# Kernel optimization log

Measured on AMD Instinct MI355X. Metric: run time of the kernel, lower is better.

## Reference

```python
import jax, jax.numpy as jnp
import numpy as np

# Orthonormal (integral-normalized) real spherical harmonics, l = 0..3,
# components ordered [Y_0^0, Y_1^{-1..1}, Y_2^{-2..2}, Y_3^{-3..3}],
# with the e3nn/cuEquivariance l=1 ordering (y, z, x).
_C00 = float(0.5 * np.sqrt(1.0 / np.pi))
_C1 = float(np.sqrt(3.0 / (4.0 * np.pi)))
_C2m2 = float(0.5 * np.sqrt(15.0 / np.pi))
_C20 = float(0.25 * np.sqrt(5.0 / np.pi))
_C22 = float(0.25 * np.sqrt(15.0 / np.pi))
_C3m3 = float(0.25 * np.sqrt(35.0 / (2.0 * np.pi)))
_C3m2 = float(0.5 * np.sqrt(105.0 / np.pi))
_C3m1 = float(0.25 * np.sqrt(21.0 / (2.0 * np.pi)))
_C30 = float(0.25 * np.sqrt(7.0 / np.pi))
_C32 = float(0.25 * np.sqrt(105.0 / np.pi))

N_EDGES = 4_000_000


def setup_inputs() -> dict:
    key = jax.random.key(0)
    vectors = jax.random.normal(key, (N_EDGES, 3), dtype=jnp.float32)
    return {"vectors": vectors}


def _sh_l3(vectors):
    # normalize=True: project onto unit sphere first
    v = vectors * jax.lax.rsqrt(jnp.sum(vectors * vectors, axis=-1, keepdims=True))
    x, y, z = v[..., 0], v[..., 1], v[..., 2]
    x2, y2, z2 = x * x, y * y, z * z
    one = jnp.ones_like(x)
    ys = [
        _C00 * one,                       # l=0
        _C1 * y, _C1 * z, _C1 * x,        # l=1 (m=-1,0,1)
        _C2m2 * x * y,                    # l=2, m=-2
        _C2m2 * y * z,                    # l=2, m=-1
        _C20 * (3.0 * z2 - 1.0),          # l=2, m=0
        _C2m2 * x * z,                    # l=2, m=1
        _C22 * (x2 - y2),                 # l=2, m=2
        _C3m3 * y * (3.0 * x2 - y2),      # l=3, m=-3
        _C3m2 * x * y * z,                # l=3, m=-2
        _C3m1 * y * (5.0 * z2 - 1.0),     # l=3, m=-1
        _C30 * z * (5.0 * z2 - 3.0),      # l=3, m=0
        _C3m1 * x * (5.0 * z2 - 1.0),     # l=3, m=1
        _C32 * z * (x2 - y2),             # l=3, m=2
        _C3m3 * x * (x2 - 3.0 * y2),      # l=3, m=3
    ]
    return jnp.stack(ys, axis=-1)  # (..., 16)


def reference(vectors) -> jnp.ndarray:
    return _sh_l3(vectors)
```

## Files before the change

kernel.cpp:

```cpp
#include <hip/hip_runtime.h>

#define C00  0.28209479177387814f
#define C1   0.4886025119029199f
#define C2M2 1.0925484305920792f
#define C20  0.31539156525252005f
#define C22  0.5462742152960396f
#define C3M3 0.5900435899266435f
#define C3M2 2.890611442640554f
#define C3M1 0.4570457994644658f
#define C30  0.3731763325901154f
#define C32  1.445305721320277f

typedef float vfloat4 __attribute__((ext_vector_type(4)));

#define NBLOCKS 2048

__global__ __launch_bounds__(256) void sh_l3_kernel(
    const float* __restrict__ v, float* __restrict__ out, int ntiles) {
    __shared__ float vin[2][768];

    const int t = threadIdx.x;
    const unsigned c = t & 3u;
    const unsigned esub = t >> 2;

    const vfloat4* v4 = reinterpret_cast<const vfloat4*>(v);
    vfloat4* out4 = reinterpret_cast<vfloat4*>(out);

    unsigned tile = blockIdx.x;
    if (tile < (unsigned)ntiles && t < 192)
        reinterpret_cast<vfloat4*>(vin[0])[t] = v4[192u * tile + t];
    __syncthreads();

    for (unsigned i = 0; tile < (unsigned)ntiles; tile += NBLOCKS, ++i) {
        const unsigned cur = i & 1u;

        const unsigned nxt = tile + NBLOCKS;
        if (nxt < (unsigned)ntiles && t < 192)
            reinterpret_cast<vfloat4*>(vin[cur ^ 1u])[t] = v4[192u * nxt + t];

        const unsigned long long obase = 1024ull * tile;
        #pragma unroll
        for (int k = 0; k < 4; ++k) {
            const unsigned e = (unsigned)k * 64u + esub;
            float x = vin[cur][3u * e + 0u];
            float y = vin[cur][3u * e + 1u];
            float z = vin[cur][3u * e + 2u];

            float rinv = rsqrtf(x * x + y * y + z * z);
            x *= rinv; y *= rinv; z *= rinv;
            float x2 = x * x, y2 = y * y, z2 = z * z;

            vfloat4 o0, o1, o2, o3;
            o0.x = C00;
            o0.y = C1 * y;
            o0.z = C1 * z;
            o0.w = C1 * x;
            o1.x = C2M2 * x * y;
            o1.y = C2M2 * y * z;
            o1.z = C20 * (3.0f * z2 - 1.0f);
            o1.w = C2M2 * x * z;
            o2.x = C22 * (x2 - y2);
            o2.y = C3M3 * y * (3.0f * x2 - y2);
            o2.z = C3M2 * x * y * z;
            o2.w = C3M1 * y * (5.0f * z2 - 1.0f);
            o3.x = C30 * z * (5.0f * z2 - 3.0f);
            o3.y = C3M1 * x * (5.0f * z2 - 1.0f);
            o3.z = C32 * z * (x2 - y2);
            o3.w = C3M3 * x * (x2 - 3.0f * y2);

            vfloat4 w = o0;
            w = (c == 1u) ? o1 : w;
            w = (c == 2u) ? o2 : w;
            w = (c == 3u) ? o3 : w;

            __builtin_nontemporal_store(w, &out4[obase + (unsigned)k * 256u + (unsigned)t]);
        }
        __syncthreads();
    }
}

extern "C" void kernel_launch(void* const* d_in, const int* in_sizes, int n_in,
                              void* d_out, int out_size, void* d_ws, size_t ws_size,
                              hipStream_t stream) {
    const float* v = (const float*)d_in[0];
    float* out = (float*)d_out;
    int n = in_sizes[0] / 3;
    int ntiles = n / 256;
    int grid = ntiles < NBLOCKS ? ntiles : NBLOCKS;
    sh_l3_kernel<<<grid, 256, 0, stream>>>(v, out, ntiles);
}
```

Baseline: 282.8 us.

## Preload all tile inputs into registers and redistribute via wave shuffles

Replaces the double-buffered shared-memory staging loop with an up-front load of up to eight tiles of xyz into registers per thread. Each thread normalizes its own vector once, and the values reach the four output lanes through __shfl, which removes the redundant rsqrt per component lane and all __syncthreads. The loads are now strided scalar float loads instead of vec4 loads, and MAXIT=8 assumes ntiles <= 8*NBLOCKS. Larger inputs would silently drop tiles.

```diff
diff --git a/kernel.cpp b/kernel.cpp
--- a/kernel.cpp
+++ b/kernel.cpp
@@ -14,68 +14,73 @@
 typedef float vfloat4 __attribute__((ext_vector_type(4)));
 
 #define NBLOCKS 2048
+#define MAXIT   8
 
 __global__ __launch_bounds__(256) void sh_l3_kernel(
     const float* __restrict__ v, float* __restrict__ out, int ntiles) {
-    __shared__ float vin[2][768];
+    const int t = threadIdx.x;
+    const int w = t >> 6;
+    const int l = t & 63;
+    const int eo = ((l >> 4) << 6) + (w << 4) + (l & 15);
+    const int c = l & 3;
 
-    const int t = threadIdx.x;
-    const unsigned c = t & 3u;
-    const unsigned esub = t >> 2;
+    float xs[MAXIT], ys[MAXIT], zs[MAXIT];
 
-    const vfloat4* v4 = reinterpret_cast<const vfloat4*>(v);
+    #pragma unroll
+    for (int i = 0; i < MAXIT; ++i) {
+        const unsigned tile = blockIdx.x + (unsigned)i * NBLOCKS;
+        if (tile < (unsigned)ntiles) {
+            const float* p = v + 768ull * tile + 3u * (unsigned)eo;
+            xs[i] = p[0]; ys[i] = p[1]; zs[i] = p[2];
+        }
+    }
+
     vfloat4* out4 = reinterpret_cast<vfloat4*>(out);
 
-    unsigned tile = blockIdx.x;
-    if (tile < (unsigned)ntiles && t < 192)
-        reinterpret_cast<vfloat4*>(vin[0])[t] = v4[192u * tile + t];
-    __syncthreads();
+    #pragma unroll
+    for (int i = 0; i < MAXIT; ++i) {
+        const unsigned tile = blockIdx.x + (unsigned)i * NBLOCKS;
+        if (tile >= (unsigned)ntiles) break;
 
-    for (unsigned i = 0; tile < (unsigned)ntiles; tile += NBLOCKS, ++i) {
-        const unsigned cur = i & 1u;
+        float x = xs[i], y = ys[i], z = zs[i];
+        float rinv = rsqrtf(x * x + y * y + z * z);
+        x *= rinv; y *= rinv; z *= rinv;
 
-        const unsigned nxt = tile + NBLOCKS;
-        if (nxt < (unsigned)ntiles && t < 192)
-            reinterpret_cast<vfloat4*>(vin[cur ^ 1u])[t] = v4[192u * nxt + t];
-
-        const unsigned long long obase = 1024ull * tile;
+        const unsigned obase = 1024u * tile;
         #pragma unroll
         for (int k = 0; k < 4; ++k) {
-            const unsigned e = (unsigned)k * 64u + esub;
-            float x = vin[cur][3u * e + 0u];
-            float y = vin[cur][3u * e + 1u];
-            float z = vin[cur][3u * e + 2u];
-
-            float rinv = rsqrtf(x * x + y * y + z * z);
-            x *= rinv; y *= rinv; z *= rinv;
-            float x2 = x * x, y2 = y * y, z2 = z * z;
+            const int src = (k << 4) | (l >> 2);
+            float sx = __shfl(x, src);
+            float sy = __shfl(y, src);
+            float sz = __shfl(z, src);
+            float x2 = sx * sx, y2 = sy * sy, z2 = sz * sz;
 
             vfloat4 o0, o1, o2, o3;
             o0.x = C00;
-            o0.y = C1 * y;
-            o0.z = C1 * z;
-            o0.w = C1 * x;
-            o1.x = C2M2 * x * y;
-            o1.y = C2M2 * y * z;
+            o0.y = C1 * sy;
+            o0.z = C1 * sz;
+            o0.w = C1 * sx;
+            o1.x = C2M2 * sx * sy;
+            o1.y = C2M2 * sy * sz;
             o1.z = C20 * (3.0f * z2 - 1.0f);
-            o1.w = C2M2 * x * z;
+            o1.w = C2M2 * sx * sz;
             o2.x = C22 * (x2 - y2);
-            o2.y = C3M3 * y * (3.0f * x2 - y2);
-            o2.z = C3M2 * x * y * z;
-            o2.w = C3M1 * y * (5.0f * z2 - 1.0f);
-            o3.x = C30 * z * (5.0f * z2 - 3.0f);
-            o3.y = C3M1 * x * (5.0f * z2 - 1.0f);
-            o3.z = C32 * z * (x2 - y2);
-            o3.w = C3M3 * x * (x2 - 3.0f * y2);
+            o2.y = C3M3 * sy * (3.0f * x2 - y2);
+            o2.z = C3M2 * sx * sy * sz;
+            o2.w = C3M1 * sy * (5.0f * z2 - 1.0f);
+            o3.x = C30 * sz * (5.0f * z2 - 3.0f);
+            o3.y = C3M1 * sx * (5.0f * z2 - 1.0f);
+            o3.z = C32 * sz * (x2 - y2);
+            o3.w = C3M3 * sx * (x2 - 3.0f * y2);
 
-            vfloat4 w = o0;
-            w = (c == 1u) ? o1 : w;
-            w = (c == 2u) ? o2 : w;
-            w = (c == 3u) ? o3 : w;
+            vfloat4 wv = o0;
+            wv = (c == 1) ? o1 : wv;
+            wv = (c == 2) ? o2 : wv;
+            wv = (c == 3) ? o3 : wv;
 
-            __builtin_nontemporal_store(w, &out4[obase + (unsigned)k * 256u + (unsigned)t]);
+            __builtin_nontemporal_store(
+                wv, &out4[obase + (unsigned)(k << 8) + (unsigned)t]);
         }
-        __syncthreads();
     }
 }
 
```

Result: no change. 281.1 us (-0.6%).
